# Optimization experiments

Hardware: AMD Instinct MI355X
Metric: run time of the kernel (lower is better)

## Reference

```python
import jax, jax.numpy as jnp
import numpy as np

ALPHA = 1.0


def setup_inputs() -> dict:
    key = jax.random.key(0)
    k1, k2 = jax.random.split(key)
    N, D, K = 262144, 256, 256
    x = jax.random.normal(k1, (N, D), dtype=jnp.float32)
    clusters = jax.random.normal(k2, (K, D), dtype=jnp.float32)
    return {"x": x, "clusters": clusters}


def reference(x, clusters):
    # Squared euclidean distance to each cluster center without materializing
    x_sq = jnp.sum(x * x, axis=1, keepdims=True)            # (N, 1)
    c_sq = jnp.sum(clusters * clusters, axis=1)[None, :]    # (1, K)
    cross = jnp.einsum('nd,kd->nk', x, clusters)            # (N, K)
    sq_dist = x_sq - 2.0 * cross + c_sq                     # (N, K)
    # Student-t kernel (as in t-SNE / DEC): q_ij = (1 + d^2/alpha)^(-(alpha+1)/2)
    q = 1.0 / (1.0 + sq_dist / ALPHA)
    q = q ** ((ALPHA + 1.0) / 2.0)
    # Row-normalize to soft assignment probabilities.
    q = q / jnp.sum(q, axis=1, keepdims=True)
    return q
```

## Files before the change

### kernel.cpp

```cpp
#include <hip/hip_runtime.h>
#include <hip/hip_bf16.h>


#define NROWS 262144
#define DDIM  256
#define KCL   256
#define TPB   16
#define GRID  (NROWS / 64 / TPB)

using f32x4  = __attribute__((ext_vector_type(4))) float;
using s16x8  = __attribute__((ext_vector_type(8))) short;

__device__ inline unsigned short f2bf(float f) {
    unsigned int u = __float_as_uint(f);
    u += 0x7fffu + ((u >> 16) & 1u);
    return (unsigned short)(u >> 16);
}

__device__ inline short bfc(float f) {
    return (short)__bfloat16_as_ushort(__float2bfloat16(f));
}

__global__ void prep_kernel(const float* __restrict__ clusters,
                            unsigned short* __restrict__ cb,
                            float* __restrict__ csq) {
    int k    = blockIdx.x;
    int lane = threadIdx.x;
    const float* row = clusters + (size_t)k * DDIM;
    float4 a = *reinterpret_cast<const float4*>(row + lane * 4);
    ushort4 b;
    b.x = f2bf(a.x); b.y = f2bf(a.y); b.z = f2bf(a.z); b.w = f2bf(a.w);
    *reinterpret_cast<ushort4*>(cb + (size_t)k * DDIM + lane * 4) = b;
    float ss = a.x*a.x + a.y*a.y + a.z*a.z + a.w*a.w;
    #pragma unroll
    for (int m = 1; m < 64; m <<= 1) ss += __shfl_xor(ss, m);
    if (lane == 0) csq[k] = ss;
}

__global__ __launch_bounds__(512, 2) void fused_kernel(
    const float* __restrict__ x,
    const unsigned short* __restrict__ cb,
    const float* __restrict__ csq,
    float* __restrict__ out) {

    __shared__ char  lds_b[KCL * DDIM * 2];
    __shared__ float ls_sum[TPB][2][4][16];
    __shared__ int   ls_flag[2][4];

    const int tid  = threadIdx.x;
    const int lane = tid & 63;
    const int wave = tid >> 6;
    const int rg   = wave >> 1;
    const int ch   = wave & 1;
    const int c15  = lane & 15;
    const int kch  = lane >> 4;

    const int tile0 = blockIdx.x * TPB;

    #pragma unroll
    for (int it = 0; it < 16; ++it) {
        int slot = it * 8192 + tid * 16;
        int src  = slot ^ (((slot >> 9) & 7) << 4);
        __builtin_amdgcn_global_load_lds(
            (const __attribute__((address_space(1))) unsigned int*)((const char*)cb + src),
            (__attribute__((address_space(3))) unsigned int*)(lds_b + slot),
            16, 0, 0);
    }

    if (tid < 8) ((int*)ls_flag)[tid] = 0;

    float cs[8];
    #pragma unroll
    for (int f = 0; f < 8; ++f) cs[f] = csq[ch * 128 + f * 16 + c15];

    __syncthreads();

    auto xrow = [&](int t) -> const float* {
        return x + (size_t)((tile0 + t) * 64 + rg * 16 + c15) * DDIM + kch * 8;
    };

    f32x4 xv1[8], xv2[8];

    {
        const float* xr = xrow(0);
        #pragma unroll
        for (int i = 0; i < 8; ++i)
            xv1[i] = *reinterpret_cast<const f32x4*>(xr + (i >> 1) * 32 + (i & 1) * 4);
        #pragma unroll
        for (int i = 0; i < 8; ++i) {
            int ii = 8 + i;
            xv2[i] = *reinterpret_cast<const f32x4*>(xr + (ii >> 1) * 32 + (ii & 1) * 4);
        }
    }

    #pragma unroll 1
    for (int t = 0; t < TPB; ++t) {
        const int trow = (tile0 + t) * 64;

        s16x8 afrag[8];
        float p[4] = {0.f, 0.f, 0.f, 0.f};

        #pragma unroll
        for (int s4 = 0; s4 < 4; ++s4) {
            f32x4 xa = xv1[2 * s4], xb = xv1[2 * s4 + 1];
            float t0 = xa[0]*xa[0] + xa[1]*xa[1];
            float t1 = xa[2]*xa[2] + xa[3]*xa[3];
            float t2 = xb[0]*xb[0] + xb[1]*xb[1];
            float t3 = xb[2]*xb[2] + xb[3]*xb[3];
            p[s4] += (t0 + t1) + (t2 + t3);
            afrag[s4][0] = bfc(xa[0]); afrag[s4][1] = bfc(xa[1]);
            afrag[s4][2] = bfc(xa[2]); afrag[s4][3] = bfc(xa[3]);
            afrag[s4][4] = bfc(xb[0]); afrag[s4][5] = bfc(xb[1]);
            afrag[s4][6] = bfc(xb[2]); afrag[s4][7] = bfc(xb[3]);
        }

        f32x4 acc[8];
        #pragma unroll
        for (int f = 0; f < 8; ++f) acc[f] = (f32x4){0.f, 0.f, 0.f, 0.f};

        __builtin_amdgcn_s_setprio(1);
        #pragma unroll
        for (int s = 0; s < 4; ++s) {
            #pragma unroll
            for (int f = 0; f < 8; ++f) {
                int ba = ((ch * 128 + f * 16 + c15) * 512) + s * 64 + kch * 16;
                ba ^= ((c15 & 7) << 4);
                s16x8 bfrag = *reinterpret_cast<const s16x8*>(lds_b + ba);
                acc[f] = __builtin_amdgcn_mfma_f32_16x16x32_bf16(afrag[s], bfrag,
                                                                 acc[f], 0, 0, 0);
            }
        }
        __builtin_amdgcn_s_setprio(0);

        #pragma unroll
        for (int s4 = 0; s4 < 4; ++s4) {
            f32x4 xa = xv2[2 * s4], xb = xv2[2 * s4 + 1];
            float t0 = xa[0]*xa[0] + xa[1]*xa[1];
            float t1 = xa[2]*xa[2] + xa[3]*xa[3];
            float t2 = xb[0]*xb[0] + xb[1]*xb[1];
            float t3 = xb[2]*xb[2] + xb[3]*xb[3];
            p[s4] += (t0 + t1) + (t2 + t3);
            int s = 4 + s4;
            afrag[s][0] = bfc(xa[0]); afrag[s][1] = bfc(xa[1]);
            afrag[s][2] = bfc(xa[2]); afrag[s][3] = bfc(xa[3]);
            afrag[s][4] = bfc(xb[0]); afrag[s][5] = bfc(xb[1]);
            afrag[s][6] = bfc(xb[2]); afrag[s][7] = bfc(xb[3]);
        }

        if (t + 1 < TPB) {
            const float* xn = xrow(t + 1);
            #pragma unroll
            for (int i = 0; i < 8; ++i)
                xv1[i] = *reinterpret_cast<const f32x4*>(xn + (i >> 1) * 32 + (i & 1) * 4);
        }

        __builtin_amdgcn_s_setprio(1);
        #pragma unroll
        for (int s = 4; s < 8; ++s) {
            #pragma unroll
            for (int f = 0; f < 8; ++f) {
                int ba = ((ch * 128 + f * 16 + c15) * 512) + s * 64 + kch * 16;
                ba ^= ((c15 & 7) << 4);
                s16x8 bfrag = *reinterpret_cast<const s16x8*>(lds_b + ba);
                acc[f] = __builtin_amdgcn_mfma_f32_16x16x32_bf16(afrag[s], bfrag,
                                                                 acc[f], 0, 0, 0);
            }
        }
        __builtin_amdgcn_s_setprio(0);

        float xsq = (p[0] + p[1]) + (p[2] + p[3]);
        xsq += __shfl_xor(xsq, 16);
        xsq += __shfl_xor(xsq, 32);

        float psum[4];
        #pragma unroll
        for (int r = 0; r < 4; ++r) {
            float xrr = __shfl(xsq, kch * 4 + r);
            float s = 0.f;
            #pragma unroll
            for (int f = 0; f < 8; ++f) {
                float d2 = xrr - 2.0f * acc[f][r] + cs[f];
                float qv = __builtin_amdgcn_rcpf(1.0f + d2);
                acc[f][r] = qv;
                s += qv;
            }
            s += __shfl_xor(s, 1);
            s += __shfl_xor(s, 2);
            s += __shfl_xor(s, 4);
            s += __shfl_xor(s, 8);
            psum[r] = s;
        }

        if (c15 == 0) {
            #pragma unroll
            for (int r = 0; r < 4; ++r)
                ls_sum[t][ch][rg][kch * 4 + r] = psum[r];
        }
        asm volatile("s_waitcnt lgkmcnt(0)" ::: "memory");
        if (lane == 0)
            __atomic_store_n(&ls_flag[ch][rg], t + 1, __ATOMIC_RELAXED);

        if (t + 1 < TPB) {
            const float* xn = xrow(t + 1);
            #pragma unroll
            for (int i = 0; i < 8; ++i) {
                int ii = 8 + i;
                xv2[i] = *reinterpret_cast<const f32x4*>(xn + (ii >> 1) * 32 + (ii & 1) * 4);
            }
        }

        volatile int* pf = (volatile int*)&ls_flag[ch ^ 1][rg];
        while (*pf <= t) { __builtin_amdgcn_s_sleep(1); }
        asm volatile("" ::: "memory");

        const int row0t = trow + rg * 16;
        #pragma unroll
        for (int r = 0; r < 4; ++r) {
            float other = ls_sum[t][ch ^ 1][rg][kch * 4 + r];
            float inv = __builtin_amdgcn_rcpf(psum[r] + other);
            const size_t orow = (size_t)(row0t + kch * 4 + r) * KCL;
            #pragma unroll
            for (int f = 0; f < 8; ++f) {
                __builtin_nontemporal_store(acc[f][r] * inv,
                                            &out[orow + ch * 128 + f * 16 + c15]);
            }
        }
    }
}

extern "C" void kernel_launch(void* const* d_in, const int* in_sizes, int n_in,
                              void* d_out, int out_size, void* d_ws, size_t ws_size,
                              hipStream_t stream) {
    const float* x        = (const float*)d_in[0];
    const float* clusters = (const float*)d_in[1];
    float* out = (float*)d_out;

    unsigned short* cb  = (unsigned short*)d_ws;
    float*          csq = (float*)((char*)d_ws + (size_t)KCL * DDIM * sizeof(unsigned short));

    prep_kernel<<<KCL, 64, 0, stream>>>(clusters, cb, csq);
    fused_kernel<<<GRID, 512, 0, stream>>>(x, cb, csq, out);
}
```

Measured before the change: 127.7 us.

## Swap MFMA operands to transpose accumulator layout for vectorized row stores

Swaps the A and B operands of the MFMA so each lane's accumulator holds four consecutive cluster columns of one x row instead of four rows. The row sum then needs only two cross-lane shuffles, and each output chunk is written as a 16-byte vector store rather than scalar stores. Cluster norms move into LDS so they can be read as vectors in the new layout. The xv2 prefetch for the next tile is removed; those loads now happen at the top of each iteration, which may expose global load latency.

```diff
diff --git a/kernel.cpp b/kernel.cpp
--- a/kernel.cpp
+++ b/kernel.cpp
@@ -44,6 +44,7 @@
     float* __restrict__ out) {
 
     __shared__ char  lds_b[KCL * DDIM * 2];
+    __shared__ float ls_csq[KCL];
     __shared__ float ls_sum[TPB][2][4][16];
     __shared__ int   ls_flag[2][4];
 
@@ -66,12 +67,8 @@
             (__attribute__((address_space(3))) unsigned int*)(lds_b + slot),
             16, 0, 0);
     }
-
+    if (tid < KCL) ls_csq[tid] = csq[tid];
     if (tid < 8) ((int*)ls_flag)[tid] = 0;
-
-    float cs[8];
-    #pragma unroll
-    for (int f = 0; f < 8; ++f) cs[f] = csq[ch * 128 + f * 16 + c15];
 
     __syncthreads();
 
@@ -86,16 +83,18 @@
         #pragma unroll
         for (int i = 0; i < 8; ++i)
             xv1[i] = *reinterpret_cast<const f32x4*>(xr + (i >> 1) * 32 + (i & 1) * 4);
+    }
+
+    #pragma unroll 1
+    for (int t = 0; t < TPB; ++t) {
+        const int trow = (tile0 + t) * 64;
+        const float* xr = xrow(t);
+
         #pragma unroll
         for (int i = 0; i < 8; ++i) {
             int ii = 8 + i;
             xv2[i] = *reinterpret_cast<const f32x4*>(xr + (ii >> 1) * 32 + (ii & 1) * 4);
         }
-    }
-
-    #pragma unroll 1
-    for (int t = 0; t < TPB; ++t) {
-        const int trow = (tile0 + t) * 64;
 
         s16x8 afrag[8];
         float p[4] = {0.f, 0.f, 0.f, 0.f};
@@ -126,7 +125,7 @@
                 int ba = ((ch * 128 + f * 16 + c15) * 512) + s * 64 + kch * 16;
                 ba ^= ((c15 & 7) << 4);
                 s16x8 bfrag = *reinterpret_cast<const s16x8*>(lds_b + ba);
-                acc[f] = __builtin_amdgcn_mfma_f32_16x16x32_bf16(afrag[s], bfrag,
+                acc[f] = __builtin_amdgcn_mfma_f32_16x16x32_bf16(bfrag, afrag[s],
                                                                  acc[f], 0, 0, 0);
             }
         }
@@ -162,7 +161,7 @@
                 int ba = ((ch * 128 + f * 16 + c15) * 512) + s * 64 + kch * 16;
                 ba ^= ((c15 & 7) << 4);
                 s16x8 bfrag = *reinterpret_cast<const s16x8*>(lds_b + ba);
-                acc[f] = __builtin_amdgcn_mfma_f32_16x16x32_bf16(afrag[s], bfrag,
+                acc[f] = __builtin_amdgcn_mfma_f32_16x16x32_bf16(bfrag, afrag[s],
                                                                  acc[f], 0, 0, 0);
             }
         }
@@ -172,58 +171,39 @@
         xsq += __shfl_xor(xsq, 16);
         xsq += __shfl_xor(xsq, 32);
 
-        float psum[4];
-        #pragma unroll
-        for (int r = 0; r < 4; ++r) {
-            float xrr = __shfl(xsq, kch * 4 + r);
-            float s = 0.f;
-            #pragma unroll
-            for (int f = 0; f < 8; ++f) {
-                float d2 = xrr - 2.0f * acc[f][r] + cs[f];
+        float srow = 0.f;
+        #pragma unroll
+        for (int f = 0; f < 8; ++f) {
+            f32x4 cq = *reinterpret_cast<const f32x4*>(&ls_csq[ch * 128 + f * 16 + kch * 4]);
+            #pragma unroll
+            for (int r = 0; r < 4; ++r) {
+                float d2 = xsq - 2.0f * acc[f][r] + cq[r];
                 float qv = __builtin_amdgcn_rcpf(1.0f + d2);
                 acc[f][r] = qv;
-                s += qv;
+                srow += qv;
             }
-            s += __shfl_xor(s, 1);
-            s += __shfl_xor(s, 2);
-            s += __shfl_xor(s, 4);
-            s += __shfl_xor(s, 8);
-            psum[r] = s;
-        }
-
-        if (c15 == 0) {
-            #pragma unroll
-            for (int r = 0; r < 4; ++r)
-                ls_sum[t][ch][rg][kch * 4 + r] = psum[r];
-        }
+        }
+        srow += __shfl_xor(srow, 16);
+        srow += __shfl_xor(srow, 32);
+
+        if (kch == 0) ls_sum[t][ch][rg][c15] = srow;
         asm volatile("s_waitcnt lgkmcnt(0)" ::: "memory");
         if (lane == 0)
             __atomic_store_n(&ls_flag[ch][rg], t + 1, __ATOMIC_RELAXED);
 
-        if (t + 1 < TPB) {
-            const float* xn = xrow(t + 1);
-            #pragma unroll
-            for (int i = 0; i < 8; ++i) {
-                int ii = 8 + i;
-                xv2[i] = *reinterpret_cast<const f32x4*>(xn + (ii >> 1) * 32 + (ii & 1) * 4);
-            }
-        }
-
         volatile int* pf = (volatile int*)&ls_flag[ch ^ 1][rg];
         while (*pf <= t) { __builtin_amdgcn_s_sleep(1); }
         asm volatile("" ::: "memory");
 
-        const int row0t = trow + rg * 16;
-        #pragma unroll
-        for (int r = 0; r < 4; ++r) {
-            float other = ls_sum[t][ch ^ 1][rg][kch * 4 + r];
-            float inv = __builtin_amdgcn_rcpf(psum[r] + other);
-            const size_t orow = (size_t)(row0t + kch * 4 + r) * KCL;
-            #pragma unroll
-            for (int f = 0; f < 8; ++f) {
-                __builtin_nontemporal_store(acc[f][r] * inv,
-                                            &out[orow + ch * 128 + f * 16 + c15]);
-            }
+        float other = ls_sum[t][ch ^ 1][rg][c15];
+        float inv = __builtin_amdgcn_rcpf(srow + other);
+
+        const size_t obase = (size_t)(trow + rg * 16 + c15) * KCL + ch * 128 + kch * 4;
+        #pragma unroll
+        for (int f = 0; f < 8; ++f) {
+            f32x4 v = { acc[f][0] * inv, acc[f][1] * inv,
+                        acc[f][2] * inv, acc[f][3] * inv };
+            __builtin_nontemporal_store(v, reinterpret_cast<f32x4*>(out + obase + f * 16));
         }
     }
 }
```

Result: slower. 138.6 us (+8.5%).
